# Kernel tuning notes

Measured on AMD Instinct MI355X. Metric: run time of the kernel, lower is better.

The kernel has to match this reference:

```python
import jax, jax.numpy as jnp
import numpy as np

K_H, K_W = 3, 3
STRIDE, PAD = 1, 1
GN_GROUPS = 32
EPS = 1e-5


def setup_inputs() -> dict:
    key = jax.random.key(0)
    k1, k2, k3 = jax.random.split(key, 3)
    B, C, H, W = 4, 256, 64, 64
    Cout = 256
    x = jax.random.normal(k1, (B, C, H, W), jnp.float32)
    offset = jax.random.normal(k2, (B, 2 * K_H * K_W, H, W), jnp.float32)
    weight = jax.random.normal(k3, (Cout, C, K_H, K_W), jnp.float32) * 0.02
    gamma = jnp.ones((Cout,), jnp.float32)
    beta = jnp.zeros((Cout,), jnp.float32)
    return {"x": x, "offset": offset, "weight": weight, "gamma": gamma, "beta": beta}


def _deform_conv(x, offset, weight):
    B, C, H, W = x.shape
    Cout = weight.shape[0]
    K = K_H * K_W
    Ho = (H + 2 * PAD - K_H) // STRIDE + 1
    Wo = (W + 2 * PAD - K_W) // STRIDE + 1
    ky, kx = jnp.meshgrid(jnp.arange(K_H), jnp.arange(K_W), indexing='ij')
    ky = ky.reshape(K).astype(x.dtype)
    kx = kx.reshape(K).astype(x.dtype)
    # base sampling positions per kernel tap
    py_base = (jnp.arange(Ho) * STRIDE - PAD).astype(x.dtype)[None, :] + ky[:, None]  # [K,Ho]
    px_base = (jnp.arange(Wo) * STRIDE - PAD).astype(x.dtype)[None, :] + kx[:, None]  # [K,Wo]
    off = offset.reshape(B, K, 2, Ho, Wo)  # mmcv layout: (dy, dx) pairs per tap
    py = py_base[None, :, :, None] + off[:, :, 0]  # [B,K,Ho,Wo]
    px = px_base[None, :, None, :] + off[:, :, 1]  # [B,K,Ho,Wo]
    y0 = jnp.floor(py)
    x0 = jnp.floor(px)
    ly = py - y0
    lx = px - x0
    xf = x.reshape(B, C, H * W)

    def gather(yi, xi):
        valid = (yi >= 0) & (yi <= H - 1) & (xi >= 0) & (xi <= W - 1)
        yc = jnp.clip(yi, 0, H - 1).astype(jnp.int32)
        xc = jnp.clip(xi, 0, W - 1).astype(jnp.int32)
        idx = yc * W + xc  # [B,K,Ho,Wo]
        vals = jax.vmap(lambda xb, ib: xb[:, ib])(xf, idx)  # [B,C,K,Ho,Wo]
        return vals * valid[:, None].astype(x.dtype)

    g00 = gather(y0, x0)
    g01 = gather(y0, x0 + 1)
    g10 = gather(y0 + 1, x0)
    g11 = gather(y0 + 1, x0 + 1)
    wy = ly[:, None]  # [B,1,K,Ho,Wo]
    wx = lx[:, None]
    val = ((1 - wy) * (1 - wx) * g00 + (1 - wy) * wx * g01
           + wy * (1 - wx) * g10 + wy * wx * g11)  # [B,C,K,Ho,Wo]
    return jnp.einsum('bckhw,ock->bohw', val, weight.reshape(Cout, C, K))


def reference(x, offset, weight, gamma, beta):
    y = _deform_conv(x, offset, weight)  # [B,Cout,Ho,Wo]
    B, C, H, W = y.shape
    yg = y.reshape(B, GN_GROUPS, C // GN_GROUPS, H, W)
    mean = jnp.mean(yg, axis=(2, 3, 4), keepdims=True)
    var = jnp.var(yg, axis=(2, 3, 4), keepdims=True)
    yn = ((yg - mean) * jax.lax.rsqrt(var + EPS)).reshape(B, C, H, W)
    out = yn * gamma[None, :, None, None] + beta[None, :, None, None]
    return jax.nn.relu(out)
```

## Files before the change

### kernel.cpp

```cpp
#include <hip/hip_runtime.h>

typedef unsigned short ushort_t;
typedef __bf16 bf16x8 __attribute__((ext_vector_type(8)));
typedef float f32x4 __attribute__((ext_vector_type(4)));
typedef void __attribute__((address_space(1))) gvoid_t;
typedef void __attribute__((address_space(3))) lvoid_t;

__device__ __forceinline__ float bflo(unsigned u) { return __builtin_bit_cast(float, u << 16); }
__device__ __forceinline__ float bfhi(unsigned u) { return __builtin_bit_cast(float, u & 0xffff0000u); }
__device__ __forceinline__ unsigned f2bf_bits(float f) {
  unsigned u = __builtin_bit_cast(unsigned, f);
  return (u + 0x7fffu + ((u >> 16) & 1u)) >> 16;
}
__device__ __forceinline__ ushort_t f2bf(float f) { return (ushort_t)f2bf_bits(f); }

__global__ __launch_bounds__(256) void k_prep(const float* __restrict__ x,
                                              const float* __restrict__ w,
                                              ushort_t* __restrict__ xt,
                                              ushort_t* __restrict__ wb,
                                              float* __restrict__ stats) {
  const int gid = blockIdx.x;
  const int t = threadIdx.x;
  if (gid >= 1024) {
    if (gid == 1024) stats[t] = 0.f;
    const int idx = (gid - 1024) * 256 + t;
    const float* src = w + (size_t)idx * 9;
    const float4 a = *(const float4*)(src);
    const float4 b4 = *(const float4*)(src + 4);
    const float c8v = src[8];
    wb[(0 << 16) + idx] = f2bf(a.x);
    wb[(1 << 16) + idx] = f2bf(a.y);
    wb[(2 << 16) + idx] = f2bf(a.z);
    wb[(3 << 16) + idx] = f2bf(a.w);
    wb[(4 << 16) + idx] = f2bf(b4.x);
    wb[(5 << 16) + idx] = f2bf(b4.y);
    wb[(6 << 16) + idx] = f2bf(b4.z);
    wb[(7 << 16) + idx] = f2bf(b4.w);
    wb[(8 << 16) + idx] = f2bf(c8v);
    return;
  }
  __shared__ __attribute__((aligned(16))) ushort_t tile[64][68];
  const int b = gid >> 8;
  const int ct = (gid >> 6) & 3;
  const int pt = gid & 63;
  const float* xb = x + ((size_t)(b * 256 + ct * 64)) * 4096 + pt * 64;
  #pragma unroll
  for (int i = 0; i < 4; ++i) {
    const int idx = t + 256 * i;
    const int c_l = idx >> 4;
    const int p4 = (idx & 15) * 4;
    const float4 v = *(const float4*)(xb + (size_t)c_l * 4096 + p4);
    uint2 pk;
    pk.x = f2bf_bits(v.x) | (f2bf_bits(v.y) << 16);
    pk.y = f2bf_bits(v.z) | (f2bf_bits(v.w) << 16);
    *(uint2*)&tile[c_l][p4] = pk;
  }
  __syncthreads();
  ushort_t* xo = xt + ((size_t)(b * 4096 + pt * 64)) * 256 + ct * 64;
  #pragma unroll
  for (int i = 0; i < 2; ++i) {
    const int u = t + 256 * i;
    const int p_l = u >> 3;
    const int c8 = u & 7;
    uint4 r;
    r.x = (unsigned)tile[c8 * 8 + 0][p_l] | ((unsigned)tile[c8 * 8 + 1][p_l] << 16);
    r.y = (unsigned)tile[c8 * 8 + 2][p_l] | ((unsigned)tile[c8 * 8 + 3][p_l] << 16);
    r.z = (unsigned)tile[c8 * 8 + 4][p_l] | ((unsigned)tile[c8 * 8 + 5][p_l] << 16);
    r.w = (unsigned)tile[c8 * 8 + 6][p_l] | ((unsigned)tile[c8 * 8 + 7][p_l] << 16);
    *(uint4*)(xo + (size_t)p_l * 256 + c8 * 8) = r;
  }
}

struct SMeta {
  float w00, w01, w10, w11;
  int i00, i01, i10, i11;
};
__device__ __forceinline__ SMeta meta_for(int h, int gw, int k, float oy, float ox) {
  SMeta m;
  const float py = (float)(h - 1 + k / 3) + oy;
  const float px = (float)(gw - 1 + k % 3) + ox;
  const float fy = floorf(py), fx = floorf(px);
  const float ly = py - fy, lx = px - fx;
  const int iy0 = (int)fy, ix0 = (int)fx;
  const float vy0 = (iy0 >= 0 && iy0 < 64) ? 1.f : 0.f;
  const float vy1 = (iy0 >= -1 && iy0 < 63) ? 1.f : 0.f;
  const float vx0 = (ix0 >= 0 && ix0 < 64) ? 1.f : 0.f;
  const float vx1 = (ix0 >= -1 && ix0 < 63) ? 1.f : 0.f;
  m.w00 = (1.f - ly) * (1.f - lx) * vy0 * vx0;
  m.w01 = (1.f - ly) * lx * vy0 * vx1;
  m.w10 = ly * (1.f - lx) * vy1 * vx0;
  m.w11 = ly * lx * vy1 * vx1;
  const int cy0 = min(max(iy0, 0), 63), cy1 = min(max(iy0 + 1, 0), 63);
  const int cx0 = min(max(ix0, 0), 63), cx1 = min(max(ix0 + 1, 0), 63);
  m.i00 = (cy0 * 64 + cx0) * 256;
  m.i01 = (cy0 * 64 + cx1) * 256;
  m.i10 = (cy1 * 64 + cx0) * 256;
  m.i11 = (cy1 * 64 + cx1) * 256;
  return m;
}

__device__ __forceinline__ unsigned lerp_pack(unsigned a, unsigned b, unsigned c, unsigned d,
                                              float w00, float w01, float w10, float w11) {
  float lo = w00 * bflo(a) + w01 * bflo(b) + w10 * bflo(c) + w11 * bflo(d);
  float hi = w00 * bfhi(a) + w01 * bfhi(b) + w10 * bfhi(c) + w11 * bfhi(d);
  return f2bf_bits(lo) | (f2bf_bits(hi) << 16);
}

template <int KH>
__device__ __forceinline__ void run_gemm(const float* __restrict__ offb,
                                         const ushort_t* __restrict__ xtb,
                                         const ushort_t* __restrict__ wb,
                                         ushort_t* Ab, ushort_t* Bb,
                                         int h, int s_w, int c8, int t,
                                         int wm, int wn, int wq, int wr,
                                         f32x4 (&acc)[2][4]) {
  float oy[5], ox[5];
  #pragma unroll
  for (int i = 0; i < 5; ++i) {
    oy[i] = offb[(2 * (KH * 4 + i)) * 4096];
    ox[i] = offb[(2 * (KH * 4 + i) + 1) * 4096];
  }

#define GATHER(N)                                                \
  {                                                              \
    const int c_ = KH * 18 + (N);                                \
    const int tap_ = c_ >> 2;                                    \
    const int loc_ = tap_ - KH * 4;                              \
    const int c0_ = (c_ & 3) << 6;                               \
    m = meta_for(h, s_w, tap_, oy[loc_], ox[loc_]);              \
    const int cc_ = c0_ + c8 * 8;                                \
    q00 = *(const uint4*)(xtb + m.i00 + cc_);                    \
    q01 = *(const uint4*)(xtb + m.i01 + cc_);                    \
    q10 = *(const uint4*)(xtb + m.i10 + cc_);                    \
    q11 = *(const uint4*)(xtb + m.i11 + cc_);                    \
  }

#define B_ISSUE(N, BUF)                                                                        \
  {                                                                                            \
    const int c_ = KH * 18 + (N);                                                              \
    const int tap_ = c_ >> 2;                                                                  \
    const int c0_ = (c_ & 3) << 6;                                                             \
    _Pragma("unroll") for (int i_ = 0; i_ < 4; ++i_) {                                         \
      const int idx_ = i_ * 512 + t;                                                           \
      const int row_ = idx_ >> 3, slot_ = idx_ & 7;                                            \
      const ushort_t* g_ = wb + (tap_ << 16) + row_ * 256 + c0_ + ((slot_ ^ (row_ & 7)) << 3); \
      __builtin_amdgcn_global_load_lds(                                                        \
          (gvoid_t*)g_, (lvoid_t*)((char*)Bb + (BUF) * 32768 + idx_ * 16), 16, 0, 0);          \
    }                                                                                          \
  }

#define A_WRITE(BUF)                                                         \
  {                                                                          \
    uint4 r;                                                                 \
    r.x = lerp_pack(q00.x, q01.x, q10.x, q11.x, m.w00, m.w01, m.w10, m.w11); \
    r.y = lerp_pack(q00.y, q01.y, q10.y, q11.y, m.w00, m.w01, m.w10, m.w11); \
    r.z = lerp_pack(q00.z, q01.z, q10.z, q11.z, m.w00, m.w01, m.w10, m.w11); \
    r.w = lerp_pack(q00.w, q01.w, q10.w, q11.w, m.w00, m.w01, m.w10, m.w11); \
    *(uint4*)&Ab[(BUF) * 4096 + s_w * 64 + ((c8 ^ (s_w & 7)) << 3)] = r;     \
  }

  {
    SMeta m;
    uint4 q00, q01, q10, q11;
    B_ISSUE(0, 0);
    GATHER(0);
    A_WRITE(0);
  }
  __syncthreads();

  #pragma unroll
  for (int n = 0; n < 18; ++n) {
    const int cur = n & 1;
    const int nb = cur ^ 1;
    SMeta m;
    uint4 q00, q01, q10, q11;
    if (n < 17) {
      B_ISSUE(n + 1, nb);
      GATHER(n + 1);
    }
    #pragma unroll
    for (int ks = 0; ks < 2; ++ks) {
      bf16x8 af[2], bfr[4];
      #pragma unroll
      for (int tm = 0; tm < 2; ++tm) {
        const int row = wm * 32 + tm * 16 + wr;
        const int slot = (ks * 4 + wq) ^ (row & 7);
        af[tm] = *(const bf16x8*)&Ab[cur * 4096 + row * 64 + slot * 8];
      }
      #pragma unroll
      for (int tn = 0; tn < 4; ++tn) {
        const int row = wn * 64 + tn * 16 + wr;
        const int slot = (ks * 4 + wq) ^ (row & 7);
        bfr[tn] = *(const bf16x8*)&Bb[cur * 16384 + row * 64 + slot * 8];
      }
      #pragma unroll
      for (int tm = 0; tm < 2; ++tm)
        #pragma unroll
        for (int tn = 0; tn < 4; ++tn)
          acc[tm][tn] =
              __builtin_amdgcn_mfma_f32_16x16x32_bf16(af[tm], bfr[tn], acc[tm][tn], 0, 0, 0);
    }
    if (n < 17) {
      A_WRITE(nb);
      __syncthreads();
    }
  }
#undef GATHER
#undef B_ISSUE
#undef A_WRITE
}

__global__ __launch_bounds__(512) void k_gemm(const float* __restrict__ off,
                                              const ushort_t* __restrict__ xt,
                                              const ushort_t* __restrict__ wb,
                                              ushort_t* __restrict__ y0,
                                              ushort_t* __restrict__ y1) {
  __shared__ __attribute__((aligned(16))) ushort_t Abuf[2][64 * 64];
  __shared__ __attribute__((aligned(16))) ushort_t Bbuf[2][256 * 64];

  const int bid = blockIdx.x;
  const int rowid = bid & 255;
  const int kh = bid >> 8;
  const int lb = ((rowid & 7) << 5) | (rowid >> 3);
  const int b = lb >> 6;
  const int h = lb & 63;
  const int t = threadIdx.x;
  const int wave = t >> 6;
  const int lane = t & 63;
  const int wq = lane >> 4;
  const int wr = lane & 15;
  const int wm = wave >> 2;
  const int wn = wave & 3;
  const int s_w = t >> 3;
  const int c8 = t & 7;

  const f32x4 zero = {0.f, 0.f, 0.f, 0.f};
  f32x4 acc[2][4];
  #pragma unroll
  for (int i = 0; i < 2; ++i)
    #pragma unroll
    for (int j = 0; j < 4; ++j) acc[i][j] = zero;

  const ushort_t* xtb = xt + (size_t)b * 4096 * 256;
  const float* offb = off + (size_t)b * 18 * 4096 + h * 64 + s_w;

  if (kh == 0)
    run_gemm<0>(offb, xtb, wb, &Abuf[0][0], &Bbuf[0][0], h, s_w, c8, t, wm, wn, wq, wr, acc);
  else
    run_gemm<1>(offb, xtb, wb, &Abuf[0][0], &Bbuf[0][0], h, s_w, c8, t, wm, wn, wq, wr, acc);

  ushort_t* yb = (kh ? y1 : y0) + ((size_t)(b * 4096 + h * 64)) * 256;
  #pragma unroll
  for (int tm = 0; tm < 2; ++tm) {
    #pragma unroll
    for (int tn = 0; tn < 4; ++tn) {
      const int o = wn * 64 + tn * 16 + wr;
      #pragma unroll
      for (int r2 = 0; r2 < 4; ++r2) {
        const int ww = wm * 32 + tm * 16 + wq * 4 + r2;
        yb[ww * 256 + o] = f2bf(acc[tm][tn][r2]);
      }
    }
  }
}

__global__ __launch_bounds__(256) void k_comb(const ushort_t* __restrict__ y0,
                                              const ushort_t* __restrict__ y1,
                                              ushort_t* __restrict__ yc,
                                              float* __restrict__ stats) {
  __shared__ float tile[64][65];
  const int bid = blockIdx.x;
  const int lb = ((bid & 7) << 7) | (bid >> 3);
  const int b = lb >> 8;
  const int st = (lb >> 2) & 63;
  const int ot = lb & 3;
  const int t = threadIdx.x;
  const size_t ybase = ((size_t)(b * 4096 + st * 64)) * 256 + ot * 64;
  float sum = 0.f, ss = 0.f;
  #pragma unroll
  for (int i = 0; i < 2; ++i) {
    const int u = t + 256 * i;
    const int s_l = u >> 3;
    const int o8 = u & 7;
    const size_t adr = ybase + (size_t)s_l * 256 + o8 * 8;
    const uint4 a = *(const uint4*)(y0 + adr);
    const uint4 c = *(const uint4*)(y1 + adr);
    float v[8];
    v[0] = bflo(a.x) + bflo(c.x); v[1] = bfhi(a.x) + bfhi(c.x);
    v[2] = bflo(a.y) + bflo(c.y); v[3] = bfhi(a.y) + bfhi(c.y);
    v[4] = bflo(a.z) + bflo(c.z); v[5] = bfhi(a.z) + bfhi(c.z);
    v[6] = bflo(a.w) + bflo(c.w); v[7] = bfhi(a.w) + bfhi(c.w);
    #pragma unroll
    for (int j = 0; j < 8; ++j) {
      sum += v[j];
      ss += v[j] * v[j];
      tile[s_l][o8 * 8 + j] = v[j];
    }
  }
  #pragma unroll
  for (int d = 8; d < 64; d <<= 1) {
    sum += __shfl_xor(sum, d, 64);
    ss += __shfl_xor(ss, d, 64);
  }
  if ((t & 63) < 8) {
    const int g = ot * 8 + (t & 7);
    atomicAdd(&stats[(b * 32 + g) * 2], sum);
    atomicAdd(&stats[(b * 32 + g) * 2 + 1], ss);
  }
  __syncthreads();
  #pragma unroll
  for (int i = 0; i < 2; ++i) {
    const int u = t + 256 * i;
    const int o_l = u >> 3;
    const int s8 = u & 7;
    float v[8];
    #pragma unroll
    for (int j = 0; j < 8; ++j) v[j] = tile[s8 * 8 + j][o_l];
    uint4 r;
    r.x = f2bf_bits(v[0]) | (f2bf_bits(v[1]) << 16);
    r.y = f2bf_bits(v[2]) | (f2bf_bits(v[3]) << 16);
    r.z = f2bf_bits(v[4]) | (f2bf_bits(v[5]) << 16);
    r.w = f2bf_bits(v[6]) | (f2bf_bits(v[7]) << 16);
    *(uint4*)(yc + ((size_t)(b * 256 + ot * 64 + o_l)) * 4096 + st * 64 + s8 * 8) = r;
  }
}

__global__ __launch_bounds__(256) void k_apply(const ushort_t* __restrict__ yc,
                                               const float* __restrict__ stats,
                                               const float* __restrict__ gamma,
                                               const float* __restrict__ beta,
                                               float* __restrict__ out) {
  const int bid = blockIdx.x;
  const int lb = ((bid & 7) << 8) | (bid >> 3);
  const size_t base = (size_t)lb * 2048 + threadIdx.x * 8;
  const int b = (int)(base >> 20);
  const int o = (int)((base >> 12) & 255);
  const int g = o >> 3;
  const float s1 = stats[(b * 32 + g) * 2];
  const float s2 = stats[(b * 32 + g) * 2 + 1];
  const float mean = s1 * (1.f / 32768.f);
  const float var = s2 * (1.f / 32768.f) - mean * mean;
  const float rstd = rsqrtf(var + 1e-5f);
  const float sc = rstd * gamma[o];
  const float sh = beta[o] - mean * sc;
  const uint4 a = *(const uint4*)(yc + base);
  float v[8];
  v[0] = bflo(a.x); v[1] = bfhi(a.x);
  v[2] = bflo(a.y); v[3] = bfhi(a.y);
  v[4] = bflo(a.z); v[5] = bfhi(a.z);
  v[6] = bflo(a.w); v[7] = bfhi(a.w);
  float4 f0, f1;
  f0.x = fmaxf(v[0] * sc + sh, 0.f);
  f0.y = fmaxf(v[1] * sc + sh, 0.f);
  f0.z = fmaxf(v[2] * sc + sh, 0.f);
  f0.w = fmaxf(v[3] * sc + sh, 0.f);
  f1.x = fmaxf(v[4] * sc + sh, 0.f);
  f1.y = fmaxf(v[5] * sc + sh, 0.f);
  f1.z = fmaxf(v[6] * sc + sh, 0.f);
  f1.w = fmaxf(v[7] * sc + sh, 0.f);
  *(float4*)(out + base) = f0;
  *(float4*)(out + base + 4) = f1;
}

extern "C" void kernel_launch(void* const* d_in, const int* in_sizes, int n_in,
                              void* d_out, int out_size, void* d_ws, size_t ws_size,
                              hipStream_t stream) {
  const float* x = (const float*)d_in[0];
  const float* off = (const float*)d_in[1];
  const float* w = (const float*)d_in[2];
  const float* gamma = (const float*)d_in[3];
  const float* beta = (const float*)d_in[4];
  float* out = (float*)d_out;

  char* ws = (char*)d_ws;
  ushort_t* y0 = (ushort_t*)(ws);
  ushort_t* y1 = (ushort_t*)(ws + 8388608);
  ushort_t* xt = (ushort_t*)(ws + 16777216);
  ushort_t* yc = xt;
  ushort_t* wb = (ushort_t*)(ws + 25165824);
  float* stats = (float*)(ws + 26345472);

  k_prep<<<1280, 256, 0, stream>>>(x, w, xt, wb, stats);
  k_gemm<<<512, 512, 0, stream>>>(off, xt, wb, y0, y1);
  k_comb<<<1024, 256, 0, stream>>>(y0, y1, yc, stats);
  k_apply<<<2048, 256, 0, stream>>>(yc, stats, gamma, beta, out);
}
```

Baseline: 81.05 us.

## Split deformable-conv GEMM K dimension into three tap groups with halved K-chunks

The GEMM kernel's K-split grows from two partial sums (by tap half) to three (three taps each), so 768 blocks launch instead of 512. The K-chunk per iteration is halved to 32 channels, which halves LDS buffers, and only half the threads do the bilinear gathering. The third partial result is staged in the output buffer and summed in the combine kernel. The aim is better occupancy and GPU fill, at the cost of an extra partial-sum write and read and more barrier iterations.

```diff
diff --git a/kernel.cpp b/kernel.cpp
--- a/kernel.cpp
+++ b/kernel.cpp
@@ -106,29 +106,31 @@
   return f2bf_bits(lo) | (f2bf_bits(hi) << 16);
 }
 
-template <int KH>
+template <int KT>
 __device__ __forceinline__ void run_gemm(const float* __restrict__ offb,
                                          const ushort_t* __restrict__ xtb,
                                          const ushort_t* __restrict__ wb,
                                          ushort_t* Ab, ushort_t* Bb,
-                                         int h, int s_w, int c8, int t,
+                                         int h, int s_w, int c4, int t, bool samp,
                                          int wm, int wn, int wq, int wr,
                                          f32x4 (&acc)[2][4]) {
-  float oy[5], ox[5];
-  #pragma unroll
-  for (int i = 0; i < 5; ++i) {
-    oy[i] = offb[(2 * (KH * 4 + i)) * 4096];
-    ox[i] = offb[(2 * (KH * 4 + i) + 1) * 4096];
+  float oy[3], ox[3];
+  if (samp) {
+    #pragma unroll
+    for (int i = 0; i < 3; ++i) {
+      oy[i] = offb[(2 * (KT * 3 + i)) * 4096];
+      ox[i] = offb[(2 * (KT * 3 + i) + 1) * 4096];
+    }
   }
 
 #define GATHER(N)                                                \
   {                                                              \
-    const int c_ = KH * 18 + (N);                                \
-    const int tap_ = c_ >> 2;                                    \
-    const int loc_ = tap_ - KH * 4;                              \
-    const int c0_ = (c_ & 3) << 6;                               \
+    const int c_ = KT * 24 + (N);                                \
+    const int tap_ = c_ >> 3;                                    \
+    const int loc_ = tap_ - KT * 3;                              \
+    const int c0_ = (c_ & 7) << 5;                               \
     m = meta_for(h, s_w, tap_, oy[loc_], ox[loc_]);              \
-    const int cc_ = c0_ + c8 * 8;                                \
+    const int cc_ = c0_ + c4 * 8;                                \
     q00 = *(const uint4*)(xtb + m.i00 + cc_);                    \
     q01 = *(const uint4*)(xtb + m.i01 + cc_);                    \
     q10 = *(const uint4*)(xtb + m.i10 + cc_);                    \
@@ -137,61 +139,62 @@
 
 #define B_ISSUE(N, BUF)                                                                        \
   {                                                                                            \
-    const int c_ = KH * 18 + (N);                                                              \
-    const int tap_ = c_ >> 2;                                                                  \
-    const int c0_ = (c_ & 3) << 6;                                                             \
-    _Pragma("unroll") for (int i_ = 0; i_ < 4; ++i_) {                                         \
-      const int idx_ = i_ * 512 + t;                                                           \
-      const int row_ = idx_ >> 3, slot_ = idx_ & 7;                                            \
-      const ushort_t* g_ = wb + (tap_ << 16) + row_ * 256 + c0_ + ((slot_ ^ (row_ & 7)) << 3); \
+    const int c_ = KT * 24 + (N);                                                              \
+    const int tap_ = c_ >> 3;                                                                  \
+    const int c0_ = (c_ & 7) << 5;                                                             \
+    _Pragma("unroll") for (int i_ = 0; i_ < 2; ++i_) {                                         \
+      const int idx_ = i_ * 512 + t;                             \
+      const int row_ = idx_ >> 2, slot_ = idx_ & 3;                                            \
+      const ushort_t* g_ = wb + (tap_ << 16) + row_ * 256 + c0_ + ((slot_ ^ (row_ & 3)) << 3); \
       __builtin_amdgcn_global_load_lds(                                                        \
-          (gvoid_t*)g_, (lvoid_t*)((char*)Bb + (BUF) * 32768 + idx_ * 16), 16, 0, 0);          \
+          (gvoid_t*)g_, (lvoid_t*)((char*)Bb + (BUF) * 16384 + idx_ * 16), 16, 0, 0);          \
     }                                                                                          \
   }
 
-#define A_WRITE(BUF)                                                         \
-  {                                                                          \
-    uint4 r;                                                                 \
-    r.x = lerp_pack(q00.x, q01.x, q10.x, q11.x, m.w00, m.w01, m.w10, m.w11); \
-    r.y = lerp_pack(q00.y, q01.y, q10.y, q11.y, m.w00, m.w01, m.w10, m.w11); \
-    r.z = lerp_pack(q00.z, q01.z, q10.z, q11.z, m.w00, m.w01, m.w10, m.w11); \
-    r.w = lerp_pack(q00.w, q01.w, q10.w, q11.w, m.w00, m.w01, m.w10, m.w11); \
-    *(uint4*)&Ab[(BUF) * 4096 + s_w * 64 + ((c8 ^ (s_w & 7)) << 3)] = r;     \
+#define A_WRITE(BUF)                                                           \
+  {                                                                            \
+    uint4 r;                                                                   \
+    r.x = lerp_pack(q00.x, q01.x, q10.x, q11.x, m.w00, m.w01, m.w10, m.w11);   \
+    r.y = lerp_pack(q00.y, q01.y, q10.y, q11.y, m.w00, m.w01, m.w10, m.w11);   \
+    r.z = lerp_pack(q00.z, q01.z, q10.z, q11.z, m.w00, m.w01, m.w10, m.w11);   \
+    r.w = lerp_pack(q00.w, q01.w, q10.w, q11.w, m.w00, m.w01, m.w10, m.w11);   \
+    *(uint4*)&Ab[(BUF) * 2048 + s_w * 32 + ((c4 ^ (s_w & 3)) << 3)] = r;       \
   }
 
   {
     SMeta m;
     uint4 q00, q01, q10, q11;
     B_ISSUE(0, 0);
-    GATHER(0);
-    A_WRITE(0);
+    if (samp) {
+      GATHER(0);
+      A_WRITE(0);
+    }
   }
   __syncthreads();
 
   #pragma unroll
-  for (int n = 0; n < 18; ++n) {
+  for (int n = 0; n < 24; ++n) {
     const int cur = n & 1;
     const int nb = cur ^ 1;
     SMeta m;
     uint4 q00, q01, q10, q11;
-    if (n < 17) {
+    if (n < 23) {
       B_ISSUE(n + 1, nb);
-      GATHER(n + 1);
-    }
-    #pragma unroll
-    for (int ks = 0; ks < 2; ++ks) {
+      if (samp) GATHER(n + 1);
+    }
+    {
       bf16x8 af[2], bfr[4];
       #pragma unroll
       for (int tm = 0; tm < 2; ++tm) {
         const int row = wm * 32 + tm * 16 + wr;
-        const int slot = (ks * 4 + wq) ^ (row & 7);
-        af[tm] = *(const bf16x8*)&Ab[cur * 4096 + row * 64 + slot * 8];
+        const int slot = wq ^ (row & 3);
+        af[tm] = *(const bf16x8*)&Ab[cur * 2048 + row * 32 + slot * 8];
       }
       #pragma unroll
       for (int tn = 0; tn < 4; ++tn) {
         const int row = wn * 64 + tn * 16 + wr;
-        const int slot = (ks * 4 + wq) ^ (row & 7);
-        bfr[tn] = *(const bf16x8*)&Bb[cur * 16384 + row * 64 + slot * 8];
+        const int slot = wq ^ (row & 3);
+        bfr[tn] = *(const bf16x8*)&Bb[cur * 8192 + row * 32 + slot * 8];
       }
       #pragma unroll
       for (int tm = 0; tm < 2; ++tm)
@@ -200,8 +203,8 @@
           acc[tm][tn] =
               __builtin_amdgcn_mfma_f32_16x16x32_bf16(af[tm], bfr[tn], acc[tm][tn], 0, 0, 0);
     }
-    if (n < 17) {
-      A_WRITE(nb);
+    if (n < 23) {
+      if (samp) A_WRITE(nb);
       __syncthreads();
     }
   }
@@ -214,13 +217,14 @@
                                               const ushort_t* __restrict__ xt,
                                               const ushort_t* __restrict__ wb,
                                               ushort_t* __restrict__ y0,
-                                              ushort_t* __restrict__ y1) {
-  __shared__ __attribute__((aligned(16))) ushort_t Abuf[2][64 * 64];
-  __shared__ __attribute__((aligned(16))) ushort_t Bbuf[2][256 * 64];
+                                              ushort_t* __restrict__ y1,
+                                              ushort_t* __restrict__ y2) {
+  __shared__ __attribute__((aligned(16))) ushort_t Abuf[2][64 * 32];
+  __shared__ __attribute__((aligned(16))) ushort_t Bbuf[2][256 * 32];
 
   const int bid = blockIdx.x;
   const int rowid = bid & 255;
-  const int kh = bid >> 8;
+  const int kt = bid >> 8;
   const int lb = ((rowid & 7) << 5) | (rowid >> 3);
   const int b = lb >> 6;
   const int h = lb & 63;
@@ -231,8 +235,9 @@
   const int wr = lane & 15;
   const int wm = wave >> 2;
   const int wn = wave & 3;
-  const int s_w = t >> 3;
-  const int c8 = t & 7;
+  const bool samp = (t < 256);
+  const int s_w = (t >> 2) & 63;
+  const int c4 = t & 3;
 
   const f32x4 zero = {0.f, 0.f, 0.f, 0.f};
   f32x4 acc[2][4];
@@ -244,12 +249,14 @@
   const ushort_t* xtb = xt + (size_t)b * 4096 * 256;
   const float* offb = off + (size_t)b * 18 * 4096 + h * 64 + s_w;
 
-  if (kh == 0)
-    run_gemm<0>(offb, xtb, wb, &Abuf[0][0], &Bbuf[0][0], h, s_w, c8, t, wm, wn, wq, wr, acc);
+  if (kt == 0)
+    run_gemm<0>(offb, xtb, wb, &Abuf[0][0], &Bbuf[0][0], h, s_w, c4, t, samp, wm, wn, wq, wr, acc);
+  else if (kt == 1)
+    run_gemm<1>(offb, xtb, wb, &Abuf[0][0], &Bbuf[0][0], h, s_w, c4, t, samp, wm, wn, wq, wr, acc);
   else
-    run_gemm<1>(offb, xtb, wb, &Abuf[0][0], &Bbuf[0][0], h, s_w, c8, t, wm, wn, wq, wr, acc);
-
-  ushort_t* yb = (kh ? y1 : y0) + ((size_t)(b * 4096 + h * 64)) * 256;
+    run_gemm<2>(offb, xtb, wb, &Abuf[0][0], &Bbuf[0][0], h, s_w, c4, t, samp, wm, wn, wq, wr, acc);
+
+  ushort_t* yb = (kt == 0 ? y0 : kt == 1 ? y1 : y2) + ((size_t)(b * 4096 + h * 64)) * 256;
   #pragma unroll
   for (int tm = 0; tm < 2; ++tm) {
     #pragma unroll
@@ -266,6 +273,7 @@
 
 __global__ __launch_bounds__(256) void k_comb(const ushort_t* __restrict__ y0,
                                               const ushort_t* __restrict__ y1,
+                                              const ushort_t* __restrict__ y2,
                                               ushort_t* __restrict__ yc,
                                               float* __restrict__ stats) {
   __shared__ float tile[64][65];
@@ -285,11 +293,12 @@
     const size_t adr = ybase + (size_t)s_l * 256 + o8 * 8;
     const uint4 a = *(const uint4*)(y0 + adr);
     const uint4 c = *(const uint4*)(y1 + adr);
+    const uint4 d = *(const uint4*)(y2 + adr);
     float v[8];
-    v[0] = bflo(a.x) + bflo(c.x); v[1] = bfhi(a.x) + bfhi(c.x);
-    v[2] = bflo(a.y) + bflo(c.y); v[3] = bfhi(a.y) + bfhi(c.y);
-    v[4] = bflo(a.z) + bflo(c.z); v[5] = bfhi(a.z) + bfhi(c.z);
-    v[6] = bflo(a.w) + bflo(c.w); v[7] = bfhi(a.w) + bfhi(c.w);
+    v[0] = bflo(a.x) + bflo(c.x) + bflo(d.x); v[1] = bfhi(a.x) + bfhi(c.x) + bfhi(d.x);
+    v[2] = bflo(a.y) + bflo(c.y) + bflo(d.y); v[3] = bfhi(a.y) + bfhi(c.y) + bfhi(d.y);
+    v[4] = bflo(a.z) + bflo(c.z) + bflo(d.z); v[5] = bfhi(a.z) + bfhi(c.z) + bfhi(d.z);
+    v[6] = bflo(a.w) + bflo(c.w) + bflo(d.w); v[7] = bfhi(a.w) + bfhi(c.w) + bfhi(d.w);
     #pragma unroll
     for (int j = 0; j < 8; ++j) {
       sum += v[j];
@@ -379,9 +388,10 @@
   ushort_t* yc = xt;
   ushort_t* wb = (ushort_t*)(ws + 25165824);
   float* stats = (float*)(ws + 26345472);
+  ushort_t* y2 = (ushort_t*)d_out;
 
   k_prep<<<1280, 256, 0, stream>>>(x, w, xt, wb, stats);
-  k_gemm<<<512, 512, 0, stream>>>(off, xt, wb, y0, y1);
-  k_comb<<<1024, 256, 0, stream>>>(y0, y1, yc, stats);
+  k_gemm<<<768, 512, 0, stream>>>(off, xt, wb, y0, y1, y2);
+  k_comb<<<1024, 256, 0, stream>>>(y0, y1, y2, yc, stats);
   k_apply<<<2048, 256, 0, stream>>>(yc, stats, gamma, beta, out);
 }
```

New measurement: 89.16 us. 1.1x slower.
